# Performance work log

Hardware: AMD Instinct MI355X
Metric: run time of the kernel (lower is better)

The kernel has to match this reference:

```python
import jax, jax.numpy as jnp
import numpy as np

B, N, A, O, D, Q, H = 64, 4, 1024, 128, 256, 256, 128
NEG_INF = -1e30


def setup_inputs() -> dict:
    key = jax.random.key(0)
    ks = jax.random.split(key, 8)
    q = jax.random.normal(ks[0], (B, N, 1, Q), dtype=jnp.float32)
    att1 = jax.random.uniform(ks[1], (B, N, A, O), dtype=jnp.float32)
    obj_reps = jax.random.normal(ks[2], (B, O, D), dtype=jnp.float32)
    tags_attention = jax.random.randint(ks[3], (B, N, A), 0, 2, dtype=jnp.int32)
    W1 = jax.random.normal(ks[4], (D + Q, H), dtype=jnp.float32) / np.sqrt(D + Q)
    b1 = jnp.zeros((H,), dtype=jnp.float32)
    W2 = jax.random.normal(ks[5], (H, 1), dtype=jnp.float32) / np.sqrt(H)
    b2 = jnp.zeros((1,), dtype=jnp.float32)
    return {"q": q, "att1": att1, "obj_reps": obj_reps,
            "tags_attention": tags_attention,
            "W1": W1, "b1": b1, "W2": W2, "b2": b2, "t": 1}


def reference(q, att1, obj_reps, tags_attention, W1, b1, W2, b2, t):
    # v: [B,N,A,D] = att1 [B,N,A,O] @ obj_reps [B,O,D]
    v = jnp.einsum('bnao,bod->bnad', att1, obj_reps)
    # q broadcast over token dim A, concat -> [B,N,A,D+Q]
    q_proj = jnp.broadcast_to(q, v.shape[:3] + (q.shape[-1],))
    vq = jnp.concatenate([v, q_proj], axis=-1)
    # FCNet: Linear + ReLU (dropout is identity at inference)
    joint_repr = jax.nn.relu(vq @ W1 + b1)          # [B,N,A,H]
    logits = (joint_repr @ W2 + b2)[..., 0]          # [B,N,A]
    # temperature-scaled masked softmax over tokens
    masked = jnp.where(tags_attention > 0, logits / t, NEG_INF)
    att2 = jax.nn.softmax(masked, axis=-1)           # [B,N,A]
    # attention_last: [B,N,O] = att2 [B,N,1,A] @ att1 [B,N,A,O]
    return jnp.einsum('bna,bnao->bno', att2, att1)
```

## Files before the change

kernel.cpp:

```cpp
#include <hip/hip_runtime.h>
#include <math.h>

#define Bc 64
#define Nc 4
#define Ac 1024
#define Oc 128
#define Dc 256
#define Qc 256
#define Hc 128
#define BN (Bc*Nc)

using f4     = __attribute__((ext_vector_type(4))) float;
using f32x4  = __attribute__((ext_vector_type(4))) float;
using short8 = __attribute__((ext_vector_type(8))) short;
using us4    = __attribute__((ext_vector_type(4))) unsigned short;

__device__ inline float decode_t(const void* p) {
    int i = *(const int*)p;
    if (i >= 1 && i <= 1000000) return (float)i;
    return __int_as_float(i);
}

__device__ inline unsigned short bf16_rne(float x) {
    unsigned u = __builtin_bit_cast(unsigned, x);
    u += 0x7FFFu + ((u >> 16) & 1u);
    return (unsigned short)(u >> 16);
}

__device__ inline void split_bf16(float x, unsigned short& hi, unsigned short& lo) {
    unsigned u = __builtin_bit_cast(unsigned, x);
    hi = (unsigned short)(u >> 16);
    float hif = __builtin_bit_cast(float, u & 0xFFFF0000u);
    float lof = x - hif;
    lo = (unsigned short)(__builtin_bit_cast(unsigned, lof) >> 16);
}

__global__ __launch_bounds__(256) void prep_M_kernel(
    const float* __restrict__ obj, const float* __restrict__ W1,
    unsigned short* __restrict__ Mt_hi, unsigned short* __restrict__ Mt_lo)
{
    __shared__ float w_s[32][36];
    __shared__ float obj_sT[32][68];

    const int t  = threadIdx.x;
    const int tx = t & 15;
    const int ty = t >> 4;
    const int h0 = blockIdx.x * 32;
    const int o0 = blockIdx.y * 64;
    const int b  = blockIdx.z;
    const int r8 = t >> 3, c8 = t & 7;

    const float* objb = obj + ((size_t)b * Oc + o0) * Dc;

    float acc[2][4];
    #pragma unroll
    for (int i = 0; i < 2; i++)
        #pragma unroll
        for (int j = 0; j < 4; j++) acc[i][j] = 0.f;

    f4 wv  = *(const f4*)(W1 + (size_t)r8 * Hc + h0 + c8 * 4);
    f4 ov0 = *(const f4*)(objb + (size_t)r8 * Dc + c8 * 4);
    f4 ov1 = *(const f4*)(objb + (size_t)(r8 + 32) * Dc + c8 * 4);

    for (int ko = 0; ko < 8; ++ko) {
        *(f4*)&w_s[r8][c8 * 4] = wv;
        obj_sT[c8 * 4 + 0][r8] = ov0[0];
        obj_sT[c8 * 4 + 1][r8] = ov0[1];
        obj_sT[c8 * 4 + 2][r8] = ov0[2];
        obj_sT[c8 * 4 + 3][r8] = ov0[3];
        obj_sT[c8 * 4 + 0][r8 + 32] = ov1[0];
        obj_sT[c8 * 4 + 1][r8 + 32] = ov1[1];
        obj_sT[c8 * 4 + 2][r8 + 32] = ov1[2];
        obj_sT[c8 * 4 + 3][r8 + 32] = ov1[3];
        __syncthreads();
        if (ko < 7) {
            wv  = *(const f4*)(W1 + (size_t)((ko + 1) * 32 + r8) * Hc + h0 + c8 * 4);
            ov0 = *(const f4*)(objb + (size_t)r8 * Dc + (ko + 1) * 32 + c8 * 4);
            ov1 = *(const f4*)(objb + (size_t)(r8 + 32) * Dc + (ko + 1) * 32 + c8 * 4);
        }
        #pragma unroll 4
        for (int k = 0; k < 32; k++) {
            float a0 = w_s[k][ty * 2];
            float a1 = w_s[k][ty * 2 + 1];
            f4 bv = *(const f4*)&obj_sT[k][tx * 4];
            #pragma unroll
            for (int j = 0; j < 4; j++) {
                acc[0][j] += a0 * bv[j];
                acc[1][j] += a1 * bv[j];
            }
        }
        __syncthreads();
    }

    #pragma unroll
    for (int i = 0; i < 2; i++) {
        us4 hi, lo;
        #pragma unroll
        for (int j = 0; j < 4; j++) {
            unsigned short h16, l16;
            split_bf16(acc[i][j], h16, l16);
            hi[j] = h16; lo[j] = l16;
        }
        size_t ofs = ((size_t)b * Hc + h0 + ty * 2 + i) * Oc + o0 + tx * 4;
        *(us4*)(Mt_hi + ofs) = hi;
        *(us4*)(Mt_lo + ofs) = lo;
    }
}

__global__ __launch_bounds__(512) void prep_qb_kernel(
    const float* __restrict__ q, const float* __restrict__ W1,
    const float* __restrict__ b1, float* __restrict__ qb,
    float* __restrict__ out_acc, float* __restrict__ Zsum)
{
    __shared__ float qs[256];
    __shared__ float red[4][128];
    const int t = threadIdx.x;
    const int bn = blockIdx.x;

    if (t < 256) qs[t] = q[bn * Qc + t];
    __syncthreads();

    const int h = t & 127, kq = t >> 7;
    float acc = 0.f;
    const float* w = W1 + (size_t)(Dc + kq * 64) * Hc + h;
    #pragma unroll 8
    for (int d = 0; d < 64; ++d)
        acc += qs[kq * 64 + d] * w[(size_t)d * Hc];
    red[kq][h] = acc;
    __syncthreads();

    if (t < 128) {
        qb[bn * Hc + t] = b1[t] + red[0][t] + red[1][t] + red[2][t] + red[3][t];
        out_acc[bn * Oc + t] = 0.f;
    }
    if (t == 128) Zsum[bn] = 0.f;
}

__global__ __launch_bounds__(512, 3) void main_kernel(
    const float* __restrict__ att1, const int* __restrict__ tags,
    const unsigned short* __restrict__ Mt_hi, const unsigned short* __restrict__ Mt_lo,
    const float* __restrict__ qb, const float* __restrict__ W2,
    const float* __restrict__ b2, const void* __restrict__ tptr,
    float* __restrict__ out_acc, float* __restrict__ Zsum)
{
    __shared__ unsigned short A_s[2][64][136];
    __shared__ float part2[64][9];
    __shared__ float qb_s[128], w2_s[128];
    __shared__ float e_s[64];

    const int t    = threadIdx.x;
    const int wave = t >> 6;
    const int lane = t & 63;
    const int l15  = lane & 15;
    const int quad = lane >> 4;
    const int a0 = blockIdx.x * 128;
    const int n  = blockIdx.y;
    const int b  = blockIdx.z;
    const int bn = b * Nc + n;

    const float* att_base = att1 + ((size_t)bn * Ac + a0) * Oc;

    f4 sv[4];
    #pragma unroll
    for (int s = 0; s < 4; s++) {
        int idx = t + 512 * s;
        sv[s] = *(const f4*)(att_base + (size_t)(idx >> 5) * Oc + (idx & 31) * 4);
    }

    const size_t brow = ((size_t)b * Hc + wave * 16 + l15) * Oc;
    short8 Bh[4], Bl[4];
    #pragma unroll
    for (int ks = 0; ks < 4; ks++) {
        const int ko = ks * 32 + quad * 8;
        Bh[ks] = *(const short8*)(Mt_hi + brow + ko);
        Bl[ks] = *(const short8*)(Mt_lo + brow + ko);
    }

    if (t < 128) { qb_s[t] = qb[bn * Hc + t]; w2_s[t] = W2[t]; }
    const int tag0 = (t < 64) ? tags[bn * Ac + a0 + t] : 0;
    const int tag1 = (t < 64) ? tags[bn * Ac + a0 + 64 + t] : 0;
    const float b2v  = b2[0];
    const float tval = decode_t(tptr);

    #pragma unroll
    for (int tile = 0; tile < 2; ++tile) {
        #pragma unroll
        for (int s = 0; s < 4; s++) {
            int idx = t + 512 * s;
            int r = idx >> 5, c4 = idx & 31;
            us4 h4;
            #pragma unroll
            for (int j = 0; j < 4; j++) h4[j] = bf16_rne(sv[s][j]);
            *(us4*)&A_s[tile][r][c4 * 4] = h4;
        }
        __syncthreads();

        if (tile == 0) {
            #pragma unroll
            for (int s = 0; s < 4; s++) {
                int idx = t + 512 * s;
                sv[s] = *(const f4*)(att_base + (size_t)(64 + (idx >> 5)) * Oc + (idx & 31) * 4);
            }
        }

        f32x4 acc[4];
        #pragma unroll
        for (int i = 0; i < 4; i++) acc[i] = (f32x4)(0.f);
        #pragma unroll
        for (int ks = 0; ks < 4; ks++) {
            const int ko = ks * 32 + quad * 8;
            #pragma unroll
            for (int i = 0; i < 4; i++) {
                short8 ah = *(const short8*)&A_s[tile][i * 16 + l15][ko];
                acc[i] = __builtin_amdgcn_mfma_f32_16x16x32_bf16(ah, Bh[ks], acc[i], 0, 0, 0);
                acc[i] = __builtin_amdgcn_mfma_f32_16x16x32_bf16(ah, Bl[ks], acc[i], 0, 0, 0);
            }
        }

        const int h = wave * 16 + l15;
        const float qbv = qb_s[h], w2v = w2_s[h];
        float p[4][4];
        #pragma unroll
        for (int i = 0; i < 4; i++)
            #pragma unroll
            for (int r = 0; r < 4; r++) {
                float v = acc[i][r] + qbv;
                v = v > 0.f ? v : 0.f;
                p[i][r] = v * w2v;
            }
        #pragma unroll
        for (int m = 1; m <= 8; m <<= 1)
            #pragma unroll
            for (int i = 0; i < 4; i++)
                #pragma unroll
                for (int r = 0; r < 4; r++)
                    p[i][r] += __shfl_xor(p[i][r], m);
        if (l15 == 0) {
            #pragma unroll
            for (int i = 0; i < 4; i++)
                #pragma unroll
                for (int r = 0; r < 4; r++)
                    part2[i * 16 + quad * 4 + r][wave] = p[i][r];
        }
        __syncthreads();

        if (t < 64) {
            float sum = b2v;
            #pragma unroll
            for (int x = 0; x < 8; x++) sum += part2[t][x];
            float logit = sum / tval;
            int tg = tile ? tag1 : tag0;
            float e = (tg > 0) ? __expf(logit) : 0.f;
            e_s[t] = e;
            float zs = e;
            #pragma unroll
            for (int off = 32; off > 0; off >>= 1) zs += __shfl_down(zs, off);
            if (t == 0) atomicAdd(&Zsum[bn], zs);
        }
        __syncthreads();

        const int o  = t & 127;
        const int q4 = t >> 7;
        const float* ab = att_base + ((size_t)tile * 64 + q4 * 16) * Oc + o;
        float accum = 0.f;
        #pragma unroll
        for (int a = 0; a < 16; a++)
            accum += e_s[q4 * 16 + a] * ab[(size_t)a * Oc];
        atomicAdd(&out_acc[bn * Oc + o], accum);
    }
}

__global__ void finalize_kernel(const float* __restrict__ out_acc,
                                const float* __restrict__ Zsum,
                                float* __restrict__ out)
{
    int idx = blockIdx.x * 256 + threadIdx.x;
    if (idx < BN * Oc) {
        out[idx] = out_acc[idx] / Zsum[idx >> 7];
    }
}

extern "C" void kernel_launch(void* const* d_in, const int* in_sizes, int n_in,
                              void* d_out, int out_size, void* d_ws, size_t ws_size,
                              hipStream_t stream)
{
    (void)in_sizes; (void)n_in; (void)out_size; (void)ws_size;

    const float* q    = (const float*)d_in[0];
    const float* att1 = (const float*)d_in[1];
    const float* obj  = (const float*)d_in[2];
    const int*   tags = (const int*)d_in[3];
    const float* W1   = (const float*)d_in[4];
    const float* b1   = (const float*)d_in[5];
    const float* W2   = (const float*)d_in[6];
    const float* b2   = (const float*)d_in[7];
    const void*  tptr = d_in[8];
    float* out = (float*)d_out;

    char* wsb = (char*)d_ws;
    unsigned short* Mt_hi = (unsigned short*)wsb;
    unsigned short* Mt_lo = (unsigned short*)(wsb + (size_t)2*1024*1024);
    float* qbuf = (float*)(wsb + (size_t)4*1024*1024);
    float* oacc = qbuf + (size_t)BN * Hc;
    float* Zs   = oacc + (size_t)BN * Oc;

    prep_M_kernel<<<dim3(4, 2, Bc), 256, 0, stream>>>(obj, W1, Mt_hi, Mt_lo);
    prep_qb_kernel<<<dim3(BN), 512, 0, stream>>>(q, W1, b1, qbuf, oacc, Zs);
    main_kernel<<<dim3(Ac / 128, Nc, Bc), 512, 0, stream>>>(att1, tags, Mt_hi, Mt_lo,
                                                            qbuf, W2, b2, tptr, oacc, Zs);
    finalize_kernel<<<dim3(BN * Oc / 256), 256, 0, stream>>>(oacc, Zs, out);
}
```

Before: 250.1 us.

## Process one full (b,n) row per block to drop atomics and finalize kernel

The main kernel now launches one 1024-thread block per (b,n) pair and loops over eight 128-token tiles, double-buffering the bf16 tile in LDS and prefetching the next tile's att1 and tags into registers. The softmax normaliser and the weighted sum over att1 are reduced in shared memory and registers instead of global atomics, so the separate finalize kernel and the zeroing in the prep kernel go away. In exchange the grid shrinks from 2048 to 256 blocks, each running a longer serial tile loop with more barriers per tile, which lowers parallelism and could leave CUs idle on this GPU.

```diff
diff --git a/kernel.cpp b/kernel.cpp
--- a/kernel.cpp
+++ b/kernel.cpp
@@ -109,8 +109,7 @@
 
 __global__ __launch_bounds__(512) void prep_qb_kernel(
     const float* __restrict__ q, const float* __restrict__ W1,
-    const float* __restrict__ b1, float* __restrict__ qb,
-    float* __restrict__ out_acc, float* __restrict__ Zsum)
+    const float* __restrict__ b1, float* __restrict__ qb)
 {
     __shared__ float qs[256];
     __shared__ float red[4][128];
@@ -129,45 +128,44 @@
     red[kq][h] = acc;
     __syncthreads();
 
-    if (t < 128) {
+    if (t < 128)
         qb[bn * Hc + t] = b1[t] + red[0][t] + red[1][t] + red[2][t] + red[3][t];
-        out_acc[bn * Oc + t] = 0.f;
-    }
-    if (t == 128) Zsum[bn] = 0.f;
-}
-
-__global__ __launch_bounds__(512, 3) void main_kernel(
+}
+
+__global__ __launch_bounds__(1024, 4) void main_kernel(
     const float* __restrict__ att1, const int* __restrict__ tags,
     const unsigned short* __restrict__ Mt_hi, const unsigned short* __restrict__ Mt_lo,
     const float* __restrict__ qb, const float* __restrict__ W2,
     const float* __restrict__ b2, const void* __restrict__ tptr,
-    float* __restrict__ out_acc, float* __restrict__ Zsum)
+    float* __restrict__ out)
 {
-    __shared__ unsigned short A_s[2][64][136];
-    __shared__ float part2[64][9];
+    __shared__ unsigned short A_s[2][128][136];
+    __shared__ float part2[128][9];
+    __shared__ float part3[8][132];
+    __shared__ float e_s[128];
     __shared__ float qb_s[128], w2_s[128];
-    __shared__ float e_s[64];
+    __shared__ float zfin[2];
 
     const int t    = threadIdx.x;
     const int wave = t >> 6;
     const int lane = t & 63;
     const int l15  = lane & 15;
     const int quad = lane >> 4;
-    const int a0 = blockIdx.x * 128;
-    const int n  = blockIdx.y;
-    const int b  = blockIdx.z;
-    const int bn = b * Nc + n;
-
-    const float* att_base = att1 + ((size_t)bn * Ac + a0) * Oc;
+    const int bn = blockIdx.x;
+    const int b  = bn >> 2;
+    const int rowg = (wave >> 3) * 64;
+    const int hw   = (wave & 7) * 16;
+
+    const float* att_bn = att1 + (size_t)bn * Ac * Oc;
 
     f4 sv[4];
     #pragma unroll
     for (int s = 0; s < 4; s++) {
-        int idx = t + 512 * s;
-        sv[s] = *(const f4*)(att_base + (size_t)(idx >> 5) * Oc + (idx & 31) * 4);
-    }
-
-    const size_t brow = ((size_t)b * Hc + wave * 16 + l15) * Oc;
+        int idx = t + 1024 * s;
+        sv[s] = *(const f4*)(att_bn + (size_t)idx * 4);
+    }
+
+    const size_t brow = ((size_t)b * Hc + hw + l15) * Oc;
     short8 Bh[4], Bl[4];
     #pragma unroll
     for (int ks = 0; ks < 4; ks++) {
@@ -177,30 +175,36 @@
     }
 
     if (t < 128) { qb_s[t] = qb[bn * Hc + t]; w2_s[t] = W2[t]; }
-    const int tag0 = (t < 64) ? tags[bn * Ac + a0 + t] : 0;
-    const int tag1 = (t < 64) ? tags[bn * Ac + a0 + 64 + t] : 0;
+    int tg_cur = (t < 128) ? tags[(size_t)bn * Ac + t] : 0;
     const float b2v  = b2[0];
     const float tval = decode_t(tptr);
 
-    #pragma unroll
-    for (int tile = 0; tile < 2; ++tile) {
+    float z_reg = 0.f, out_reg = 0.f;
+
+    for (int tile = 0; tile < 8; ++tile) {
+        const int buf = tile & 1;
+        const float* tile_ptr = att_bn + (size_t)tile * 128 * Oc;
+
         #pragma unroll
         for (int s = 0; s < 4; s++) {
-            int idx = t + 512 * s;
+            int idx = t + 1024 * s;
             int r = idx >> 5, c4 = idx & 31;
             us4 h4;
             #pragma unroll
             for (int j = 0; j < 4; j++) h4[j] = bf16_rne(sv[s][j]);
-            *(us4*)&A_s[tile][r][c4 * 4] = h4;
-        }
-        __syncthreads();
-
-        if (tile == 0) {
+            *(us4*)&A_s[buf][r][c4 * 4] = h4;
+        }
+        __syncthreads();
+
+        int tg_next = 0;
+        if (tile < 7) {
+            const float* np = att_bn + (size_t)(tile + 1) * 128 * Oc;
             #pragma unroll
             for (int s = 0; s < 4; s++) {
-                int idx = t + 512 * s;
-                sv[s] = *(const f4*)(att_base + (size_t)(64 + (idx >> 5)) * Oc + (idx & 31) * 4);
+                int idx = t + 1024 * s;
+                sv[s] = *(const f4*)(np + (size_t)idx * 4);
             }
+            if (t < 128) tg_next = tags[(size_t)bn * Ac + (tile + 1) * 128 + t];
         }
 
         f32x4 acc[4];
@@ -211,72 +215,83 @@
             const int ko = ks * 32 + quad * 8;
             #pragma unroll
             for (int i = 0; i < 4; i++) {
-                short8 ah = *(const short8*)&A_s[tile][i * 16 + l15][ko];
+                short8 ah = *(const short8*)&A_s[buf][rowg + i * 16 + l15][ko];
                 acc[i] = __builtin_amdgcn_mfma_f32_16x16x32_bf16(ah, Bh[ks], acc[i], 0, 0, 0);
                 acc[i] = __builtin_amdgcn_mfma_f32_16x16x32_bf16(ah, Bl[ks], acc[i], 0, 0, 0);
             }
         }
 
-        const int h = wave * 16 + l15;
-        const float qbv = qb_s[h], w2v = w2_s[h];
-        float p[4][4];
-        #pragma unroll
-        for (int i = 0; i < 4; i++)
-            #pragma unroll
-            for (int r = 0; r < 4; r++) {
-                float v = acc[i][r] + qbv;
-                v = v > 0.f ? v : 0.f;
-                p[i][r] = v * w2v;
-            }
-        #pragma unroll
-        for (int m = 1; m <= 8; m <<= 1)
+        {
+            const float qbv = qb_s[hw + l15], w2v = w2_s[hw + l15];
+            float p[4][4];
             #pragma unroll
             for (int i = 0; i < 4; i++)
                 #pragma unroll
-                for (int r = 0; r < 4; r++)
-                    p[i][r] += __shfl_xor(p[i][r], m);
-        if (l15 == 0) {
-            #pragma unroll
-            for (int i = 0; i < 4; i++)
+                for (int r = 0; r < 4; r++) {
+                    float v = acc[i][r] + qbv;
+                    v = v > 0.f ? v : 0.f;
+                    p[i][r] = v * w2v;
+                }
+            #pragma unroll
+            for (int m = 1; m <= 8; m <<= 1)
                 #pragma unroll
-                for (int r = 0; r < 4; r++)
-                    part2[i * 16 + quad * 4 + r][wave] = p[i][r];
-        }
-        __syncthreads();
-
-        if (t < 64) {
+                for (int i = 0; i < 4; i++)
+                    #pragma unroll
+                    for (int r = 0; r < 4; r++)
+                        p[i][r] += __shfl_xor(p[i][r], m);
+            if (l15 == 0) {
+                #pragma unroll
+                for (int i = 0; i < 4; i++)
+                    #pragma unroll
+                    for (int r = 0; r < 4; r++)
+                        part2[rowg + i * 16 + quad * 4 + r][wave & 7] = p[i][r];
+            }
+        }
+        __syncthreads();
+
+        if (t < 128) {
             float sum = b2v;
             #pragma unroll
             for (int x = 0; x < 8; x++) sum += part2[t][x];
             float logit = sum / tval;
-            int tg = tile ? tag1 : tag0;
-            float e = (tg > 0) ? __expf(logit) : 0.f;
+            float e = (tg_cur > 0) ? __expf(logit) : 0.f;
             e_s[t] = e;
-            float zs = e;
-            #pragma unroll
-            for (int off = 32; off > 0; off >>= 1) zs += __shfl_down(zs, off);
-            if (t == 0) atomicAdd(&Zsum[bn], zs);
-        }
-        __syncthreads();
-
-        const int o  = t & 127;
-        const int q4 = t >> 7;
-        const float* ab = att_base + ((size_t)tile * 64 + q4 * 16) * Oc + o;
-        float accum = 0.f;
-        #pragma unroll
-        for (int a = 0; a < 16; a++)
-            accum += e_s[q4 * 16 + a] * ab[(size_t)a * Oc];
-        atomicAdd(&out_acc[bn * Oc + o], accum);
-    }
-}
-
-__global__ void finalize_kernel(const float* __restrict__ out_acc,
-                                const float* __restrict__ Zsum,
-                                float* __restrict__ out)
-{
-    int idx = blockIdx.x * 256 + threadIdx.x;
-    if (idx < BN * Oc) {
-        out[idx] = out_acc[idx] / Zsum[idx >> 7];
+            z_reg += e;
+        }
+        __syncthreads();
+
+        {
+            const int o  = t & 127;
+            const int g  = t >> 7;
+            const float* ab = tile_ptr + (size_t)(g * 16) * Oc + o;
+            float accum = 0.f;
+            #pragma unroll
+            for (int a = 0; a < 16; a++)
+                accum += e_s[g * 16 + a] * ab[(size_t)a * Oc];
+            part3[g][o] = accum;
+        }
+        __syncthreads();
+
+        if (t < 128) {
+            float s = 0.f;
+            #pragma unroll
+            for (int g = 0; g < 8; g++) s += part3[g][t];
+            out_reg += s;
+        }
+        tg_cur = tg_next;
+    }
+
+    __syncthreads();
+    if (t < 128) {
+        float z = z_reg;
+        #pragma unroll
+        for (int off = 32; off > 0; off >>= 1) z += __shfl_down(z, off);
+        if (lane == 0) zfin[wave] = z;
+    }
+    __syncthreads();
+    if (t < 128) {
+        float Z = zfin[0] + zfin[1];
+        out[(size_t)bn * Oc + t] = out_reg / Z;
     }
 }
 
@@ -301,12 +316,9 @@
     unsigned short* Mt_hi = (unsigned short*)wsb;
     unsigned short* Mt_lo = (unsigned short*)(wsb + (size_t)2*1024*1024);
     float* qbuf = (float*)(wsb + (size_t)4*1024*1024);
-    float* oacc = qbuf + (size_t)BN * Hc;
-    float* Zs   = oacc + (size_t)BN * Oc;
 
     prep_M_kernel<<<dim3(4, 2, Bc), 256, 0, stream>>>(obj, W1, Mt_hi, Mt_lo);
-    prep_qb_kernel<<<dim3(BN), 512, 0, stream>>>(q, W1, b1, qbuf, oacc, Zs);
-    main_kernel<<<dim3(Ac / 128, Nc, Bc), 512, 0, stream>>>(att1, tags, Mt_hi, Mt_lo,
-                                                            qbuf, W2, b2, tptr, oacc, Zs);
-    finalize_kernel<<<dim3(BN * Oc / 256), 256, 0, stream>>>(oacc, Zs, out);
-}
+    prep_qb_kernel<<<dim3(BN), 512, 0, stream>>>(q, W1, b1, qbuf);
+    main_kernel<<<dim3(BN), 1024, 0, stream>>>(att1, tags, Mt_hi, Mt_lo,
+                                               qbuf, W2, b2, tptr, out);
+}
```

Result: no change. 248.7 us (-0.6%).
